# Kernel optimization log

Hardware: AMD Instinct MI355X
Metric: run time of the kernel (lower is better)

The kernel has to match this reference:

```python
import jax, jax.numpy as jnp
import numpy as np

B, C, H, W, N = 256, 64, 36, 36, 2000
P = H * W  # 1296 mask pixels


def setup_inputs() -> dict:
    key = jax.random.key(0)
    k1, k2, k3 = jax.random.split(key, 3)
    x = jax.random.normal(k1, (B, C, H, W), dtype=jnp.float32)
    # init_scales rows 1 and 2 give (mean=0, std=0.01) for both param tensors
    mask_weights = 0.01 * jax.random.normal(k2, (P, C, N), dtype=jnp.float32)
    readout_weights = 0.01 * jax.random.normal(k3, (C, N), dtype=jnp.float32)
    return {"x": x, "mask_weights": mask_weights, "readout_weights": readout_weights}


def reference(x, mask_weights, readout_weights):
    # x: (B, C, H, W) -> flatten spatial dims to P
    b, c, h, w = x.shape
    x_flat = x.reshape(b, c, h * w)  # (B, C, P)
    # Per-channel spatial pooling fused with weighted channel sum:
    # masked[b,c,n] = sum_p x_flat[b,c,p] * mask_weights[p,c,n]
    # out[b,n]     = sum_c masked[b,c,n] * readout_weights[c,n]
    out = jnp.einsum("bcp,pcn,cn->bn", x_flat, mask_weights, readout_weights)
    # final_relu=False => no bias / softplus
    return out
```

## Files before the change

kernel.cpp:

```cpp
#include <hip/hip_runtime.h>

typedef unsigned short ushort_t;
typedef __attribute__((ext_vector_type(8))) short bf16x8;
typedef __attribute__((ext_vector_type(4))) float f32x4;

#define C_DIM 64
#define P_DIM 1296
#define N_DIM 2000
#define B_DIM 256
#define K_DIM (C_DIM * P_DIM)
#define XB_ELEMS (B_DIM * K_DIM)
#define XB_ELEMS_PAD (XB_ELEMS + 256)
#define XB_BYTES ((size_t)XB_ELEMS_PAD * 2)
#define SLICES 32
#define OUT_ELEMS (B_DIM * N_DIM)

static __device__ __forceinline__ ushort_t f2bf(float f) {
  unsigned u = __builtin_bit_cast(unsigned, f);
  u += 0x7fffu + ((u >> 16) & 1u);
  return (ushort_t)(u >> 16);
}

__global__ void klindt_cvt_kernel(const float4* __restrict__ x,
                                  unsigned long long* __restrict__ xb) {
  int idx = blockIdx.x * 256 + threadIdx.x;
  if (idx >= XB_ELEMS_PAD / 4) return;
  unsigned long long r = 0ull;
  if (idx < XB_ELEMS / 4) {
    float4 v = x[idx];
    r = (unsigned long long)f2bf(v.x) | ((unsigned long long)f2bf(v.y) << 16) |
        ((unsigned long long)f2bf(v.z) << 32) |
        ((unsigned long long)f2bf(v.w) << 48);
  }
  xb[idx] = r;
}

__global__ void __launch_bounds__(512, 4) klindt_gemm_kernel(
    const ushort_t* __restrict__ xb, const float* __restrict__ mw,
    const float* __restrict__ rw, float* __restrict__ partials) {
  __shared__ ushort_t sA[2][8192];
  __shared__ ushort_t sB[2][4096];

  const int tid = threadIdx.x;
  const int lane = tid & 63;
  const int wid = tid >> 6;
  const int wm = wid >> 1;
  const int wn = wid & 1;
  const int n0 = blockIdx.x * 128;
  const int slice = blockIdx.y;
  const int c0 = slice * 2;

  f32x4 acc[4][4];
#pragma unroll
  for (int i = 0; i < 4; ++i)
#pragma unroll
    for (int j = 0; j < 4; ++j) {
      acc[i][j][0] = 0.f; acc[i][j][1] = 0.f;
      acc[i][j][2] = 0.f; acc[i][j][3] = 0.f;
    }

  int a_row[2], a_soff[2], a_doff[2];
#pragma unroll
  for (int it = 0; it < 2; ++it) {
    int chunk = it * 512 + tid;
    int row = chunk >> 2, t4 = chunk & 3;
    int ss = t4 ^ ((row >> 1) & 3);
    a_row[it] = row;
    a_soff[it] = ss * 8;
    a_doff[it] = chunk * 8;
  }
  int b_kq[2], b_ng[2], b_eoff[2];
#pragma unroll
  for (int it = 0; it < 2; ++it) {
    int idx = it * 512 + tid;
    int nl = idx & 15, kq = (idx >> 4) & 7, nh = idx >> 7;
    int n = nh * 16 + nl;
    b_kq[it] = kq;
    b_ng[it] = n0 + n;
    int slotp = (kq >> 1) ^ ((nl >> 1) & 3);
    b_eoff[it] = n * 32 + slotp * 8 + (kq & 1) * 4;
  }

  const int r15 = lane & 15, g4 = lane >> 4;
  const int swz = g4 ^ ((r15 >> 1) & 3);
  const int aoffbase = (wm * 64 + r15) * 32 + swz * 8;
  const int boffbase = (wn * 64 + r15) * 32 + swz * 8;

  float mv[2][4];
  float rv[2];

  auto issueA = [&](int buf, int k0) {
#pragma unroll
    for (int it = 0; it < 2; ++it) {
      const ushort_t* g = xb + (size_t)a_row[it] * K_DIM + k0 + a_soff[it];
      __builtin_amdgcn_global_load_lds(
          (const __attribute__((address_space(1))) unsigned int*)g,
          (__attribute__((address_space(3))) unsigned int*)(&sA[buf][a_doff[it]]),
          16, 0, 0);
    }
  };
  auto issueB = [&](int c, int p0) {
#pragma unroll
    for (int it = 0; it < 2; ++it) {
      const int ng = b_ng[it];
      const bool okn = ng < N_DIM;
      rv[it] = okn ? rw[c * N_DIM + ng] : 0.f;
#pragma unroll
      for (int j = 0; j < 4; ++j) {
        int p = p0 + b_kq[it] * 4 + j;
        mv[it][j] = (okn && p < P_DIM)
                        ? mw[(size_t)p * (C_DIM * N_DIM) + c * N_DIM + ng]
                        : 0.f;
      }
    }
  };
  auto writeB = [&](int buf) {
#pragma unroll
    for (int it = 0; it < 2; ++it) {
      unsigned long long pk = 0ull;
#pragma unroll
      for (int j = 0; j < 4; ++j)
        pk |= (unsigned long long)f2bf(mv[it][j] * rv[it]) << (16 * j);
      *(unsigned long long*)(&sB[buf][b_eoff[it]]) = pk;
    }
  };
  auto computeStep = [&](int buf) {
    bf16x8 bfr[4];
#pragma unroll
    for (int fn = 0; fn < 4; ++fn)
      bfr[fn] = *(const bf16x8*)(&sB[buf][boffbase + fn * 512]);
#pragma unroll
    for (int fm = 0; fm < 4; ++fm) {
      bf16x8 afr = *(const bf16x8*)(&sA[buf][aoffbase + fm * 512]);
#pragma unroll
      for (int fn = 0; fn < 4; ++fn)
        acc[fm][fn] = __builtin_amdgcn_mfma_f32_16x16x32_bf16(
            afr, bfr[fn], acc[fm][fn], 0, 0, 0);
    }
  };

  issueA(0, c0 * P_DIM);
  issueB(c0, 0);
  writeB(0);
  __syncthreads();

  const int NSTEP = 82;
  for (int s = 0; s < NSTEP; ++s) {
    int buf = s & 1;
    int s1 = s + 1;
    if (s1 < NSTEP) {
      int half = (s1 >= 41) ? 1 : 0;
      int sp = s1 - 41 * half;
      int c = c0 + half;
      issueA(buf ^ 1, c * P_DIM + sp * 32);
      issueB(c, sp * 32);
    }
    computeStep(buf);
    if (s1 < NSTEP) writeB(buf ^ 1);
    __syncthreads();
  }

  float* pb = partials + (size_t)slice * OUT_ELEMS;
#pragma unroll
  for (int fm = 0; fm < 4; ++fm) {
#pragma unroll
    for (int fn = 0; fn < 4; ++fn) {
      int nn = n0 + wn * 64 + fn * 16 + r15;
      if (nn < N_DIM) {
#pragma unroll
        for (int rr = 0; rr < 4; ++rr) {
          int m = wm * 64 + fm * 16 + g4 * 4 + rr;
          pb[m * N_DIM + nn] = acc[fm][fn][rr];
        }
      }
    }
  }
}

__global__ void klindt_reduce_kernel(const float* __restrict__ part,
                                     float* __restrict__ out) {
  int i = blockIdx.x * 256 + threadIdx.x;
  if (i < OUT_ELEMS) {
    float s = 0.f;
#pragma unroll
    for (int k = 0; k < SLICES; ++k) s += part[(size_t)k * OUT_ELEMS + i];
    out[i] = s;
  }
}

extern "C" void kernel_launch(void* const* d_in, const int* in_sizes, int n_in,
                              void* d_out, int out_size, void* d_ws,
                              size_t ws_size, hipStream_t stream) {
  (void)in_sizes; (void)n_in; (void)out_size; (void)ws_size;
  const float* x = (const float*)d_in[0];
  const float* mw = (const float*)d_in[1];
  const float* rw = (const float*)d_in[2];
  float* out = (float*)d_out;

  ushort_t* xb = (ushort_t*)d_ws;
  float* partials = (float*)((char*)d_ws + XB_BYTES);

  {
    int nvec = XB_ELEMS_PAD / 4;
    int grid = (nvec + 255) / 256;
    klindt_cvt_kernel<<<grid, 256, 0, stream>>>((const float4*)x,
                                                (unsigned long long*)xb);
  }
  {
    dim3 grid(16, SLICES);
    klindt_gemm_kernel<<<grid, 512, 0, stream>>>(xb, mw, rw, partials);
  }
  {
    int grid = (OUT_ELEMS + 255) / 256;
    klindt_reduce_kernel<<<grid, 256, 0, stream>>>(partials, out);
  }
}
```

Before: 258.9 us.

## Deepen B-load pipeline to two steps ahead with manual waitcnt barriers

Restructures the GEMM main loop so the mask-weight global loads are issued two steps ahead into alternating register sets, while the A tile is still fetched one step ahead. Each barrier now waits only for the older loads (vmcnt(8)) instead of draining everything. Addressing switches to precomputed 32-bit byte offsets, and readout weights are hoisted out of the loop. This hides more of the strided fp32 weight-load latency behind MFMA work, at the cost of more registers and fragile hand-written waitcnt counts.

New measurement: 253.0 us. 1.02x faster.

```diff
diff --git a/kernel.cpp b/kernel.cpp
--- a/kernel.cpp
+++ b/kernel.cpp
@@ -1,6 +1,7 @@
 #include <hip/hip_runtime.h>
 
 typedef unsigned short ushort_t;
+typedef unsigned int uint_t;
 typedef __attribute__((ext_vector_type(8))) short bf16x8;
 typedef __attribute__((ext_vector_type(4))) float f32x4;
 
@@ -14,6 +15,7 @@
 #define XB_BYTES ((size_t)XB_ELEMS_PAD * 2)
 #define SLICES 32
 #define OUT_ELEMS (B_DIM * N_DIM)
+#define NSTEP 82
 
 static __device__ __forceinline__ ushort_t f2bf(float f) {
   unsigned u = __builtin_bit_cast(unsigned, f);
@@ -36,7 +38,7 @@
 }
 
 __global__ void __launch_bounds__(512, 4) klindt_gemm_kernel(
-    const ushort_t* __restrict__ xb, const float* __restrict__ mw,
+    const char* __restrict__ xbb, const char* __restrict__ mwb,
     const float* __restrict__ rw, float* __restrict__ partials) {
   __shared__ ushort_t sA[2][8192];
   __shared__ ushort_t sB[2][4096];
@@ -59,26 +61,31 @@
       acc[i][j][2] = 0.f; acc[i][j][3] = 0.f;
     }
 
-  int a_row[2], a_soff[2], a_doff[2];
+  uint_t a_gbase[2]; int a_doff[2];
 #pragma unroll
   for (int it = 0; it < 2; ++it) {
     int chunk = it * 512 + tid;
     int row = chunk >> 2, t4 = chunk & 3;
     int ss = t4 ^ ((row >> 1) & 3);
-    a_row[it] = row;
-    a_soff[it] = ss * 8;
+    a_gbase[it] = (uint_t)(row * K_DIM + ss * 8) * 2u;
     a_doff[it] = chunk * 8;
   }
-  int b_kq[2], b_ng[2], b_eoff[2];
+  uint_t b_goff[2]; int b_eoff[2], b_kj[2]; bool b_ok[2];
+  float rvl[2], rvh[2];
 #pragma unroll
   for (int it = 0; it < 2; ++it) {
     int idx = it * 512 + tid;
     int nl = idx & 15, kq = (idx >> 4) & 7, nh = idx >> 7;
     int n = nh * 16 + nl;
-    b_kq[it] = kq;
-    b_ng[it] = n0 + n;
+    int ng = n0 + n;
+    bool okn = ng < N_DIM;
+    b_ok[it] = okn;
+    b_kj[it] = kq * 4;
+    b_goff[it] = (uint_t)kq * 2048000u + (uint_t)ng * 4u;
     int slotp = (kq >> 1) ^ ((nl >> 1) & 3);
     b_eoff[it] = n * 32 + slotp * 8 + (kq & 1) * 4;
+    rvl[it] = okn ? rw[c0 * N_DIM + ng] : 0.f;
+    rvh[it] = okn ? rw[(c0 + 1) * N_DIM + ng] : 0.f;
   }
 
   const int r15 = lane & 15, g4 = lane >> 4;
@@ -86,44 +93,21 @@
   const int aoffbase = (wm * 64 + r15) * 32 + swz * 8;
   const int boffbase = (wn * 64 + r15) * 32 + swz * 8;
 
-  float mv[2][4];
-  float rv[2];
-
-  auto issueA = [&](int buf, int k0) {
+  float mvE[2][4], mvO[2][4];
+
+  auto issueA = [&](int buf, int t) {
+    int half = (t >= 41) ? 1 : 0;
+    int sp = t - 41 * half;
+    uint_t kb = ((uint_t)(c0 + half) * (uint_t)P_DIM + (uint_t)sp * 32u) * 2u;
 #pragma unroll
     for (int it = 0; it < 2; ++it) {
-      const ushort_t* g = xb + (size_t)a_row[it] * K_DIM + k0 + a_soff[it];
+      const char* g = xbb + (a_gbase[it] + kb);
       __builtin_amdgcn_global_load_lds(
           (const __attribute__((address_space(1))) unsigned int*)g,
           (__attribute__((address_space(3))) unsigned int*)(&sA[buf][a_doff[it]]),
           16, 0, 0);
     }
   };
-  auto issueB = [&](int c, int p0) {
-#pragma unroll
-    for (int it = 0; it < 2; ++it) {
-      const int ng = b_ng[it];
-      const bool okn = ng < N_DIM;
-      rv[it] = okn ? rw[c * N_DIM + ng] : 0.f;
-#pragma unroll
-      for (int j = 0; j < 4; ++j) {
-        int p = p0 + b_kq[it] * 4 + j;
-        mv[it][j] = (okn && p < P_DIM)
-                        ? mw[(size_t)p * (C_DIM * N_DIM) + c * N_DIM + ng]
-                        : 0.f;
-      }
-    }
-  };
-  auto writeB = [&](int buf) {
-#pragma unroll
-    for (int it = 0; it < 2; ++it) {
-      unsigned long long pk = 0ull;
-#pragma unroll
-      for (int j = 0; j < 4; ++j)
-        pk |= (unsigned long long)f2bf(mv[it][j] * rv[it]) << (16 * j);
-      *(unsigned long long*)(&sB[buf][b_eoff[it]]) = pk;
-    }
-  };
   auto computeStep = [&](int buf) {
     bf16x8 bfr[4];
 #pragma unroll
@@ -139,26 +123,66 @@
     }
   };
 
-  issueA(0, c0 * P_DIM);
-  issueB(c0, 0);
-  writeB(0);
-  __syncthreads();
-
-  const int NSTEP = 82;
-  for (int s = 0; s < NSTEP; ++s) {
-    int buf = s & 1;
-    int s1 = s + 1;
-    if (s1 < NSTEP) {
-      int half = (s1 >= 41) ? 1 : 0;
-      int sp = s1 - 41 * half;
-      int c = c0 + half;
-      issueA(buf ^ 1, c * P_DIM + sp * 32);
-      issueB(c, sp * 32);
-    }
-    computeStep(buf);
-    if (s1 < NSTEP) writeB(buf ^ 1);
-    __syncthreads();
-  }
+#define ISSUE_B(MV, T)                                                        \
+  do {                                                                        \
+    int half_ = ((T) >= 41) ? 1 : 0;                                          \
+    int sp_ = (T)-41 * half_;                                                 \
+    uint_t ub_ = (uint_t)sp_ * 16384000u + (uint_t)(c0 + half_) * 8000u;      \
+    bool full_ = (sp_ < 40);                                                  \
+    _Pragma("unroll") for (int it_ = 0; it_ < 2; ++it_) {                     \
+      const char* bp_ = mwb + (ub_ + b_goff[it_]);                            \
+      _Pragma("unroll") for (int j_ = 0; j_ < 4; ++j_) {                      \
+        bool ok_ = b_ok[it_] && (full_ || (b_kj[it_] + j_) < 16);             \
+        MV[it_][j_] = ok_ ? *(const float*)(bp_ + (uint_t)j_ * 512000u) : 0.f;\
+      }                                                                       \
+    }                                                                         \
+  } while (0)
+
+#define WRITE_B(BUF, MV, T)                                                   \
+  do {                                                                        \
+    bool hi_ = ((T) >= 41);                                                   \
+    _Pragma("unroll") for (int it_ = 0; it_ < 2; ++it_) {                     \
+      float r_ = hi_ ? rvh[it_] : rvl[it_];                                   \
+      unsigned long long pk_ = 0ull;                                          \
+      _Pragma("unroll") for (int j_ = 0; j_ < 4; ++j_)                        \
+        pk_ |= (unsigned long long)f2bf(MV[it_][j_] * r_) << (16 * j_);       \
+      *(unsigned long long*)(&sB[BUF][b_eoff[it_]]) = pk_;                    \
+    }                                                                         \
+  } while (0)
+
+  ISSUE_B(mvE, 0);
+  issueA(0, 0);
+  WRITE_B(0, mvE, 0);
+  ISSUE_B(mvO, 1);
+  asm volatile("s_waitcnt vmcnt(8)\n\ts_waitcnt lgkmcnt(0)" ::: "memory");
+  __builtin_amdgcn_sched_barrier(0);
+  __builtin_amdgcn_s_barrier();
+  __builtin_amdgcn_sched_barrier(0);
+
+#define BODY(S, MV_ISSUE, MV_WRITE)                                           \
+  {                                                                           \
+    issueA(((S) + 1) & 1, (S) + 1);                                           \
+    ISSUE_B(MV_ISSUE, (S) + 2);                                               \
+    computeStep((S)&1);                                                       \
+    WRITE_B(((S) + 1) & 1, MV_WRITE, (S) + 1);                                \
+    asm volatile("s_waitcnt vmcnt(8)\n\ts_waitcnt lgkmcnt(0)" ::: "memory");  \
+    __builtin_amdgcn_sched_barrier(0);                                        \
+    __builtin_amdgcn_s_barrier();                                             \
+    __builtin_amdgcn_sched_barrier(0);                                        \
+  }
+
+  for (int s = 0; s < 80; s += 2) {
+    BODY(s, mvE, mvO);
+    BODY(s + 1, mvO, mvE);
+  }
+  issueA(1, 81);
+  computeStep(0);
+  WRITE_B(1, mvO, 81);
+  asm volatile("s_waitcnt vmcnt(0)\n\ts_waitcnt lgkmcnt(0)" ::: "memory");
+  __builtin_amdgcn_sched_barrier(0);
+  __builtin_amdgcn_s_barrier();
+  __builtin_amdgcn_sched_barrier(0);
+  computeStep(1);
 
   float* pb = partials + (size_t)slice * OUT_ELEMS;
 #pragma unroll
@@ -175,6 +199,9 @@
       }
     }
   }
+#undef BODY
+#undef ISSUE_B
+#undef WRITE_B
 }
 
 __global__ void klindt_reduce_kernel(const float* __restrict__ part,
@@ -193,22 +220,22 @@
                               size_t ws_size, hipStream_t stream) {
   (void)in_sizes; (void)n_in; (void)out_size; (void)ws_size;
   const float* x = (const float*)d_in[0];
-  const float* mw = (const float*)d_in[1];
+  const char* mwb = (const char*)d_in[1];
   const float* rw = (const float*)d_in[2];
   float* out = (float*)d_out;
 
-  ushort_t* xb = (ushort_t*)d_ws;
+  char* xbb = (char*)d_ws;
   float* partials = (float*)((char*)d_ws + XB_BYTES);
 
   {
     int nvec = XB_ELEMS_PAD / 4;
     int grid = (nvec + 255) / 256;
     klindt_cvt_kernel<<<grid, 256, 0, stream>>>((const float4*)x,
-                                                (unsigned long long*)xb);
+                                                (unsigned long long*)xbb);
   }
   {
     dim3 grid(16, SLICES);
-    klindt_gemm_kernel<<<grid, 512, 0, stream>>>(xb, mw, rw, partials);
+    klindt_gemm_kernel<<<grid, 512, 0, stream>>>(xbb, mwb, rw, partials);
   }
   {
     int grid = (OUT_ELEMS + 255) / 256;
```

## Split GEMM M dimension across blocks and use 32-bit byte offsets for loads

Applied to the files above, without the earlier changes.

Changes the GEMM tiling from a 256x128 tile per 512-thread block to 128x128 tiles per 256-thread block, doubling the grid so more blocks share the machine. Mask-weight loads now use precomputed 32-bit byte offsets with readout weights hoisted out of the loop, and the K-tail bounds check is confined to the last step of each channel. The cost is that each mask-weight tile is loaded and converted twice, once per M half, which doubles B-side global traffic.

Result: slower. 292.4 us (+12.9%).

```diff
diff --git a/kernel.cpp b/kernel.cpp
--- a/kernel.cpp
+++ b/kernel.cpp
@@ -1,6 +1,7 @@
 #include <hip/hip_runtime.h>
 
 typedef unsigned short ushort_t;
+typedef unsigned int uint_t;
 typedef __attribute__((ext_vector_type(8))) short bf16x8;
 typedef __attribute__((ext_vector_type(4))) float f32x4;
 
@@ -14,6 +15,7 @@
 #define XB_BYTES ((size_t)XB_ELEMS_PAD * 2)
 #define SLICES 32
 #define OUT_ELEMS (B_DIM * N_DIM)
+#define NSTEP 82
 
 static __device__ __forceinline__ ushort_t f2bf(float f) {
   unsigned u = __builtin_bit_cast(unsigned, f);
@@ -35,10 +37,10 @@
   xb[idx] = r;
 }
 
-__global__ void __launch_bounds__(512, 4) klindt_gemm_kernel(
-    const ushort_t* __restrict__ xb, const float* __restrict__ mw,
+__global__ void __launch_bounds__(256, 4) klindt_gemm_kernel(
+    const char* __restrict__ xbb, const char* __restrict__ mwb,
     const float* __restrict__ rw, float* __restrict__ partials) {
-  __shared__ ushort_t sA[2][8192];
+  __shared__ ushort_t sA[2][4096];
   __shared__ ushort_t sB[2][4096];
 
   const int tid = threadIdx.x;
@@ -46,7 +48,10 @@
   const int wid = tid >> 6;
   const int wm = wid >> 1;
   const int wn = wid & 1;
-  const int n0 = blockIdx.x * 128;
+  const int nt = blockIdx.x & 15;
+  const int mt = blockIdx.x >> 4;
+  const int n0 = nt * 128;
+  const int m0 = mt * 128;
   const int slice = blockIdx.y;
   const int c0 = slice * 2;
 
@@ -59,26 +64,31 @@
       acc[i][j][2] = 0.f; acc[i][j][3] = 0.f;
     }
 
-  int a_row[2], a_soff[2], a_doff[2];
+  uint_t a_gbase[2]; int a_doff[2];
 #pragma unroll
   for (int it = 0; it < 2; ++it) {
-    int chunk = it * 512 + tid;
+    int chunk = it * 256 + tid;
     int row = chunk >> 2, t4 = chunk & 3;
     int ss = t4 ^ ((row >> 1) & 3);
-    a_row[it] = row;
-    a_soff[it] = ss * 8;
+    a_gbase[it] = (uint_t)((m0 + row) * K_DIM + ss * 8) * 2u;
     a_doff[it] = chunk * 8;
   }
-  int b_kq[2], b_ng[2], b_eoff[2];
-#pragma unroll
-  for (int it = 0; it < 2; ++it) {
-    int idx = it * 512 + tid;
+  uint_t b_goff[4]; int b_eoff[4], b_kq[4];
+  float rvl[4], rvh[4];
+#pragma unroll
+  for (int it = 0; it < 4; ++it) {
+    int idx = it * 256 + tid;
     int nl = idx & 15, kq = (idx >> 4) & 7, nh = idx >> 7;
     int n = nh * 16 + nl;
+    int ng = n0 + n;
+    int ngc = ng < (N_DIM - 1) ? ng : (N_DIM - 1);
     b_kq[it] = kq;
-    b_ng[it] = n0 + n;
+    b_goff[it] = (uint_t)kq * 2048000u + (uint_t)ngc * 4u;
     int slotp = (kq >> 1) ^ ((nl >> 1) & 3);
     b_eoff[it] = n * 32 + slotp * 8 + (kq & 1) * 4;
+    bool okn = ng < N_DIM;
+    rvl[it] = okn ? rw[c0 * N_DIM + ng] : 0.f;
+    rvh[it] = okn ? rw[(c0 + 1) * N_DIM + ng] : 0.f;
   }
 
   const int r15 = lane & 15, g4 = lane >> 4;
@@ -86,41 +96,54 @@
   const int aoffbase = (wm * 64 + r15) * 32 + swz * 8;
   const int boffbase = (wn * 64 + r15) * 32 + swz * 8;
 
-  float mv[2][4];
-  float rv[2];
-
-  auto issueA = [&](int buf, int k0) {
+  float mv[4][4];
+
+  auto issueA = [&](int buf, int t) {
+    int half = (t >= 41) ? 1 : 0;
+    int sp = t - 41 * half;
+    uint_t kb = ((uint_t)(c0 + half) * (uint_t)P_DIM + (uint_t)sp * 32u) * 2u;
 #pragma unroll
     for (int it = 0; it < 2; ++it) {
-      const ushort_t* g = xb + (size_t)a_row[it] * K_DIM + k0 + a_soff[it];
+      const char* g = xbb + (a_gbase[it] + kb);
       __builtin_amdgcn_global_load_lds(
           (const __attribute__((address_space(1))) unsigned int*)g,
           (__attribute__((address_space(3))) unsigned int*)(&sA[buf][a_doff[it]]),
           16, 0, 0);
     }
   };
-  auto issueB = [&](int c, int p0) {
-#pragma unroll
-    for (int it = 0; it < 2; ++it) {
-      const int ng = b_ng[it];
-      const bool okn = ng < N_DIM;
-      rv[it] = okn ? rw[c * N_DIM + ng] : 0.f;
-#pragma unroll
-      for (int j = 0; j < 4; ++j) {
-        int p = p0 + b_kq[it] * 4 + j;
-        mv[it][j] = (okn && p < P_DIM)
-                        ? mw[(size_t)p * (C_DIM * N_DIM) + c * N_DIM + ng]
-                        : 0.f;
+  auto issueB = [&](int t) {
+    int half = (t >= 41) ? 1 : 0;
+    int sp = t - 41 * half;
+    uint_t ub = (uint_t)sp * 16384000u + (uint_t)(c0 + half) * 8000u;
+    if (sp < 40) {
+#pragma unroll
+      for (int it = 0; it < 4; ++it) {
+        const char* bp = mwb + (ub + b_goff[it]);
+#pragma unroll
+        for (int j = 0; j < 4; ++j)
+          mv[it][j] = *(const float*)(bp + (uint_t)j * 512000u);
       }
-    }
-  };
-  auto writeB = [&](int buf) {
-#pragma unroll
-    for (int it = 0; it < 2; ++it) {
+    } else {
+#pragma unroll
+      for (int it = 0; it < 4; ++it) {
+        const char* bp = mwb + (ub + b_goff[it]);
+#pragma unroll
+        for (int j = 0; j < 4; ++j) {
+          bool ok = (b_kq[it] * 4 + j) < 16;
+          mv[it][j] = ok ? *(const float*)(bp + (uint_t)j * 512000u) : 0.f;
+        }
+      }
+    }
+  };
+  auto writeB = [&](int buf, int t) {
+    bool hi = (t >= 41);
+#pragma unroll
+    for (int it = 0; it < 4; ++it) {
+      float r = hi ? rvh[it] : rvl[it];
       unsigned long long pk = 0ull;
 #pragma unroll
       for (int j = 0; j < 4; ++j)
-        pk |= (unsigned long long)f2bf(mv[it][j] * rv[it]) << (16 * j);
+        pk |= (unsigned long long)f2bf(mv[it][j] * r) << (16 * j);
       *(unsigned long long*)(&sB[buf][b_eoff[it]]) = pk;
     }
   };
@@ -139,26 +162,20 @@
     }
   };
 
-  issueA(0, c0 * P_DIM);
-  issueB(c0, 0);
-  writeB(0);
+  issueB(0);
+  issueA(0, 0);
+  writeB(0, 0);
   __syncthreads();
 
-  const int NSTEP = 82;
-  for (int s = 0; s < NSTEP; ++s) {
+  for (int s = 0; s < NSTEP - 1; ++s) {
     int buf = s & 1;
-    int s1 = s + 1;
-    if (s1 < NSTEP) {
-      int half = (s1 >= 41) ? 1 : 0;
-      int sp = s1 - 41 * half;
-      int c = c0 + half;
-      issueA(buf ^ 1, c * P_DIM + sp * 32);
-      issueB(c, sp * 32);
-    }
+    issueB(s + 1);
+    issueA(buf ^ 1, s + 1);
     computeStep(buf);
-    if (s1 < NSTEP) writeB(buf ^ 1);
+    writeB(buf ^ 1, s + 1);
     __syncthreads();
   }
+  computeStep((NSTEP - 1) & 1);
 
   float* pb = partials + (size_t)slice * OUT_ELEMS;
 #pragma unroll
@@ -169,7 +186,7 @@
       if (nn < N_DIM) {
 #pragma unroll
         for (int rr = 0; rr < 4; ++rr) {
-          int m = wm * 64 + fm * 16 + g4 * 4 + rr;
+          int m = m0 + wm * 64 + fm * 16 + g4 * 4 + rr;
           pb[m * N_DIM + nn] = acc[fm][fn][rr];
         }
       }
@@ -193,22 +210,22 @@
                               size_t ws_size, hipStream_t stream) {
   (void)in_sizes; (void)n_in; (void)out_size; (void)ws_size;
   const float* x = (const float*)d_in[0];
-  const float* mw = (const float*)d_in[1];
+  const char* mwb = (const char*)d_in[1];
   const float* rw = (const float*)d_in[2];
   float* out = (float*)d_out;
 
-  ushort_t* xb = (ushort_t*)d_ws;
+  char* xbb = (char*)d_ws;
   float* partials = (float*)((char*)d_ws + XB_BYTES);
 
   {
     int nvec = XB_ELEMS_PAD / 4;
     int grid = (nvec + 255) / 256;
     klindt_cvt_kernel<<<grid, 256, 0, stream>>>((const float4*)x,
-                                                (unsigned long long*)xb);
+                                                (unsigned long long*)xbb);
   }
   {
-    dim3 grid(16, SLICES);
-    klindt_gemm_kernel<<<grid, 512, 0, stream>>>(xb, mw, rw, partials);
+    dim3 grid(32, SLICES);
+    klindt_gemm_kernel<<<grid, 256, 0, stream>>>(xbb, mwb, rw, partials);
   }
   {
     int grid = (OUT_ELEMS + 255) / 256;
```
